# Kernel optimization log

Hardware: AMD Instinct MI355X
Metric: run time of the kernel (lower is better)

## Reference

```python
import jax, jax.numpy as jnp
import numpy as np

NEG_INF = -9e15


def setup_inputs() -> dict:
    key = jax.random.key(0)
    k1, k2, k3, k4, k5, k6 = jax.random.split(key, 6)
    B, N, F_IN, F_OUT = 16, 2048, 256, 128
    inputs = jax.random.normal(k1, (B, N, F_IN), dtype=jnp.float32)
    adj_matrix = jax.random.randint(k2, (B, N, N), 0, 2, dtype=jnp.int32)
    W = jax.random.normal(k3, (F_OUT, F_IN), dtype=jnp.float32) * (1.0 / np.sqrt(F_IN))
    b_W = jax.random.normal(k4, (F_OUT,), dtype=jnp.float32) * 0.02
    a = jax.random.normal(k5, (1, 2 * F_OUT), dtype=jnp.float32) * (1.0 / np.sqrt(2 * F_OUT))
    b_a = jax.random.normal(k6, (1,), dtype=jnp.float32) * 0.02
    return {"inputs": inputs, "adj_matrix": adj_matrix, "W": W, "b_W": b_W, "a": a, "b_a": b_a}


def reference(inputs, adj_matrix, W, b_W, a, b_a):
    # wh: [B, N, H]
    wh = jnp.einsum('bnf,hf->bnh', inputs, W) + b_W
    H = wh.shape[-1]
    # linear_self_W([wh_i, wh_j]) = a1.wh_i + a2.wh_j + b  (rank-1 linear over concat)
    a1 = a[0, :H]
    a2 = a[0, H:]
    src = jnp.einsum('bnh,h->bn', wh, a1)  # [B, N] contribution of row node i
    dst = jnp.einsum('bnh,h->bn', wh, a2)  # [B, N] contribution of col node j
    e = jax.nn.leaky_relu(src[:, :, None] + dst[:, None, :] + b_a[0], negative_slope=0.01)
    e = jnp.where(adj_matrix > 0, e, NEG_INF)
    att = jax.nn.softmax(e, axis=-1)  # dropout in eval mode = identity
    return jax.nn.elu(jnp.einsum('bij,bjh->bih', att, wh))
```

## Files before the change

kernel.cpp:

```cpp
#include <hip/hip_runtime.h>


#define BDIM 16
#define NDIM 2048
#define FIN 256
#define HDIM 128
#define LOG2E 1.4426950408889634f

typedef short short8 __attribute__((ext_vector_type(8)));
typedef float floatx4 __attribute__((ext_vector_type(4)));
typedef int intx4 __attribute__((ext_vector_type(4)));

__device__ __forceinline__ unsigned short f2bf(float x) {
    unsigned int u = __float_as_uint(x);
    unsigned int r = (u + 0x7fffu + ((u >> 16) & 1u)) >> 16;
    return (unsigned short)r;
}
__device__ __forceinline__ float bf2f(unsigned short s) {
    return __uint_as_float(((unsigned int)s) << 16);
}
__device__ __forceinline__ intx4 ldnt(const int* p) {
    return __builtin_nontemporal_load(reinterpret_cast<const intx4*>(p));
}

__global__ __launch_bounds__(256) void k_wh(const float* __restrict__ X,
                                            const float* __restrict__ W,
                                            const float* __restrict__ bW,
                                            const float* __restrict__ a,
                                            const float* __restrict__ ba_p,
                                            float* __restrict__ src,
                                            float* __restrict__ dst,
                                            unsigned short* __restrict__ whF) {
    __shared__ short lds[27648];
    short (*ah)[72] = (short(*)[72])lds;
    short (*al)[72] = (short(*)[72])(lds + 4608);
    short (*bh)[72] = (short(*)[72])(lds + 9216);
    short (*bl)[72] = (short(*)[72])(lds + 18432);
    short (*tb)[72] = (short(*)[72])lds;

    const int tid = threadIdx.x;
    const long row0 = (long)blockIdx.x * 64;
    const int w = tid >> 6, lane = tid & 63;
    const int lm = lane & 15, q = lane >> 4;
    const float ba0 = ba_p[0];

    float a1v[8], a2v[8], bwv[8];
    #pragma unroll
    for (int nt = 0; nt < 8; nt++) {
        a1v[nt] = a[nt * 16 + lm];
        a2v[nt] = a[HDIM + nt * 16 + lm];
        bwv[nt] = bW[nt * 16 + lm];
    }

    floatx4 acc[8];
    #pragma unroll
    for (int nt = 0; nt < 8; nt++) acc[nt] = (floatx4){0.f, 0.f, 0.f, 0.f};

    for (int k0 = 0; k0 < FIN; k0 += 64) {
        #pragma unroll
        for (int u = 0; u < 4; u++) {
            int idx = tid + u * 256;
            int r = idx >> 4, fc = (idx & 15) * 4;
            float4 v = *reinterpret_cast<const float4*>(X + (row0 + r) * FIN + k0 + fc);
            union { unsigned short s[4]; uint2 u2; } ph, pl;
            ph.s[0] = f2bf(v.x); pl.s[0] = f2bf(v.x - bf2f(ph.s[0]));
            ph.s[1] = f2bf(v.y); pl.s[1] = f2bf(v.y - bf2f(ph.s[1]));
            ph.s[2] = f2bf(v.z); pl.s[2] = f2bf(v.z - bf2f(ph.s[2]));
            ph.s[3] = f2bf(v.w); pl.s[3] = f2bf(v.w - bf2f(ph.s[3]));
            *reinterpret_cast<uint2*>(&ah[r][fc]) = ph.u2;
            *reinterpret_cast<uint2*>(&al[r][fc]) = pl.u2;
        }
        #pragma unroll
        for (int u = 0; u < 8; u++) {
            int idx = tid + u * 256;
            int hh = idx >> 4, fc = (idx & 15) * 4;
            float4 v = *reinterpret_cast<const float4*>(W + hh * FIN + k0 + fc);
            union { unsigned short s[4]; uint2 u2; } ph, pl;
            ph.s[0] = f2bf(v.x); pl.s[0] = f2bf(v.x - bf2f(ph.s[0]));
            ph.s[1] = f2bf(v.y); pl.s[1] = f2bf(v.y - bf2f(ph.s[1]));
            ph.s[2] = f2bf(v.z); pl.s[2] = f2bf(v.z - bf2f(ph.s[2]));
            ph.s[3] = f2bf(v.w); pl.s[3] = f2bf(v.w - bf2f(ph.s[3]));
            *reinterpret_cast<uint2*>(&bh[hh][fc]) = ph.u2;
            *reinterpret_cast<uint2*>(&bl[hh][fc]) = pl.u2;
        }
        __syncthreads();
        #pragma unroll
        for (int ks = 0; ks < 64; ks += 32) {
            short8 afh = *reinterpret_cast<const short8*>(&ah[w * 16 + lm][ks + q * 8]);
            short8 afl = *reinterpret_cast<const short8*>(&al[w * 16 + lm][ks + q * 8]);
            #pragma unroll
            for (int nt = 0; nt < 8; nt++) {
                short8 bfh = *reinterpret_cast<const short8*>(&bh[nt * 16 + lm][ks + q * 8]);
                short8 bfl = *reinterpret_cast<const short8*>(&bl[nt * 16 + lm][ks + q * 8]);
                acc[nt] = __builtin_amdgcn_mfma_f32_16x16x32_bf16(afh, bfh, acc[nt], 0, 0, 0);
                acc[nt] = __builtin_amdgcn_mfma_f32_16x16x32_bf16(afh, bfl, acc[nt], 0, 0, 0);
                acc[nt] = __builtin_amdgcn_mfma_f32_16x16x32_bf16(afl, bfh, acc[nt], 0, 0, 0);
            }
        }
        __syncthreads();
    }

    float s1[4] = {0.f, 0.f, 0.f, 0.f}, s2[4] = {0.f, 0.f, 0.f, 0.f};
    #pragma unroll
    for (int nt = 0; nt < 8; nt++) {
        #pragma unroll
        for (int r = 0; r < 4; r++) {
            float v = acc[nt][r] + bwv[nt];
            s1[r] += v * a1v[nt];
            s2[r] += v * a2v[nt];
            tb[nt * 16 + lm][w * 16 + q * 4 + r] = f2bf(v);
        }
    }
    #pragma unroll
    for (int r = 0; r < 4; r++) {
        #pragma unroll
        for (int o = 1; o < 16; o <<= 1) {
            s1[r] += __shfl_xor(s1[r], o);
            s2[r] += __shfl_xor(s2[r], o);
        }
    }
    if (lm == 0) {
        #pragma unroll
        for (int r = 0; r < 4; r++) {
            long row = row0 + w * 16 + q * 4 + r;
            src[row] = (s1[r] + ba0) * LOG2E;
            dst[row] = s2[r] * LOG2E;
        }
    }
    __syncthreads();
    const int b = (int)(row0 >> 11);
    const int jc0 = (int)((row0 & 2047) >> 5);
    const int f = tid >> 4;
    const int sub = tid & 15;
    const int jcrel = f >> 3, ht = f & 7;
    const size_t fbase = (((size_t)b * 64 + jc0 + jcrel) * 8 + ht) * 512;
    #pragma unroll
    for (int i = 0; i < 4; i++) {
        int l = sub * 4 + i;
        uint4 v = *reinterpret_cast<const uint4*>(&tb[ht * 16 + (l & 15)][jcrel * 32 + (l >> 4) * 8]);
        *reinterpret_cast<uint4*>(whF + fbase + l * 8) = v;
    }
}


#define MD_PRE(PW1, BK, HI)                                                    \
    do {                                                                       \
        md[PW1][0] = maskB[BK][0 + (HI)][wrow];                                \
        md[PW1][1] = maskB[BK][2 + (HI)][wrow];                                \
        md[PW1][2] = maskB[BK][4 + (HI)][wrow];                                \
        md[PW1][3] = maskB[BK][6 + (HI)][wrow];                                \
    } while (0)

#define ADJ_ISSUE(GNEXT, H)                                                    \
    do {                                                                       \
        _Pragma("unroll")                                                      \
        for (int r = 0; r < 8; r++) {                                          \
            const int* ap = adj +                                              \
                (size_t)(rowbase + cw * 16 + (H) * 8 + r) * NDIM +             \
                (GNEXT) * 256 + lane * 4;                                      \
            av[r] = ldnt(ap);                                                  \
        }                                                                      \
    } while (0)

#define ADJ_BALLOT(GNEXT, H)                                                   \
    do {                                                                       \
        _Pragma("unroll")                                                      \
        for (int r = 0; r < 8; r++) {                                          \
            unsigned long long b0 = __ballot(av[r][0] != 0);                   \
            unsigned long long b1 = __ballot(av[r][1] != 0);                   \
            unsigned long long b2 = __ballot(av[r][2] != 0);                   \
            unsigned long long b3 = __ballot(av[r][3] != 0);                   \
            if (lane < 8) {                                                    \
                unsigned long long bb = (lane < 2) ? b0                        \
                                        : (lane < 4) ? b1                      \
                                        : (lane < 6) ? b2 : b3;                \
                unsigned wv = (lane & 1) ? (unsigned)(bb >> 32) : (unsigned)bb;\
                maskB[(GNEXT) & 1][lane][cw * 16 + (H) * 8 + r] = wv;          \
            }                                                                  \
        }                                                                      \
    } while (0)

#define CHC(C)                                                                 \
    do {                                                                       \
        constexpr int PW = (C) & 1;                                            \
        const int T = g8 + (C);                                                \
        if (!(g8 == 56 && (C) == 7)) {                       \
            const float* dp = dstp + (T + 1) * 32;                             \
            d[PW ^ 1][0] = *reinterpret_cast<const floatx4*>(dp);              \
            d[PW ^ 1][1] = *reinterpret_cast<const floatx4*>(dp + 4);          \
            if ((C) < 7) {                                                     \
                MD_PRE(PW ^ 1, (g8 >> 3) & 1, (((C) + 1) & 4) ? 1 : 0);        \
            } else {                                                           \
                MD_PRE(PW ^ 1, ((g8 >> 3) + 1) & 1, 0);                        \
            }                                                                  \
        }                                                                      \
        const int base = 8 * ((C) & 3) + 2 * q;                                \
        short8 af;                                                             \
        _Pragma("unroll")                                                      \
        for (int j = 0; j < 8; j++) {                                          \
            float x = si + d[PW][j >> 2][j & 3];                               \
            x = fmaxf(x, 0.01f * x);               \
            float e2 = __builtin_amdgcn_exp2f(x);                              \
            unsigned bit = (md[PW][j & 3] >> (base + (j >> 2))) & 1u;          \
            float wgt = bit ? e2 : 0.f;                                        \
            lpart += wgt;                                                      \
            af[j] = (short)f2bf(wgt);                                          \
        }                                                                      \
        _Pragma("unroll")                                                      \
        for (int hj = 0; hj < 8; hj++) {                                       \
            short8 fb = *reinterpret_cast<const short8*>(                      \
                &whS[PW][hj * 512 + lane * 8]);                                \
            acc[hj] = __builtin_amdgcn_mfma_f32_16x16x32_bf16(af, fb,          \
                                                              acc[hj], 0, 0, 0); \
        }                                                                      \
    } while (0)

#define CHP(C)                                                                 \
    do {                                                                       \
        constexpr int PW = (C) & 1;                                            \
        const int T = g8 + (C);                                                \
        if (T + 2 < 64) {                   \
            const unsigned short* gp = gsrc + (size_t)(T + 2) * 4096;          \
            sr[PW][0] = *reinterpret_cast<const short8*>(gp);                  \
            sr[PW][1] = *reinterpret_cast<const short8*>(gp + 512);            \
        }                                                                      \
        if ((C) == 0 && g8 < 56) ADJ_ISSUE((g8 >> 3) + 1, 0);                  \
        if ((C) == 3 && g8 < 56) {                                             \
            ADJ_BALLOT((g8 >> 3) + 1, 0);                                      \
            ADJ_ISSUE((g8 >> 3) + 1, 1);                                       \
        }                                                                      \
        if ((C) == 6 && g8 < 56) ADJ_BALLOT((g8 >> 3) + 1, 1);                 \
        if (T + 1 < 64) {                 \
            *reinterpret_cast<short8*>(&whS[PW ^ 1][pofs]) = sr[PW ^ 1][0];    \
            *reinterpret_cast<short8*>(&whS[PW ^ 1][pofs + 512]) = sr[PW ^ 1][1]; \
        }                                                                      \
    } while (0)

#define ITER(C)                                                                \
    do {                                                                       \
        if (wave < 4) { CHC(C); } else { CHP(C); }                             \
        __syncthreads();                                                       \
    } while (0)

__global__ __launch_bounds__(512) void k_attn(const int* __restrict__ adj,
                                              const unsigned short* __restrict__ whF,
                                              const float* __restrict__ src,
                                              const float* __restrict__ dst,
                                              float* __restrict__ out) {
    __shared__ short whS[2][4096];
    __shared__ unsigned maskB[2][8][64];
    __shared__ float lred[64];
    __shared__ float linv_s[64];

    const int tid = threadIdx.x;
    const int bid = ((int)blockIdx.x & 7) * 64 + ((int)blockIdx.x >> 3);
    const int b = bid >> 5;
    const int i0 = (bid & 31) * 64;
    const int wave = tid >> 6, lane = tid & 63;
    const int cw = wave & 3;
    const int lm = lane & 15, q = lane >> 4;
    const int wrow = cw * 16 + lm;
    const int rowbase = b * NDIM + i0;

    const float si = src[rowbase + wrow];
    const float* dstp = dst + b * NDIM + q * 8;
    const unsigned short* gsrc =
        whF + (size_t)b * 64 * 8 * 512 + cw * 1024 + lane * 8;
    const int pofs = cw * 1024 + lane * 8;

    floatx4 acc[8];
    #pragma unroll
    for (int hj = 0; hj < 8; hj++) acc[hj] = (floatx4){0.f, 0.f, 0.f, 0.f};
    float lpart = 0.f;

    unsigned md[2][4];
    floatx4 d[2][2];
    short8 sr[2][2];
    intx4 av[8];

    if (wave >= 4) {
        short8 p0 = *reinterpret_cast<const short8*>(gsrc);
        short8 p1 = *reinterpret_cast<const short8*>(gsrc + 512);
        *reinterpret_cast<short8*>(&whS[0][pofs]) = p0;
        *reinterpret_cast<short8*>(&whS[0][pofs + 512]) = p1;
        sr[1][0] = *reinterpret_cast<const short8*>(gsrc + 4096);
        sr[1][1] = *reinterpret_cast<const short8*>(gsrc + 4096 + 512);
        ADJ_ISSUE(0, 0);
        ADJ_BALLOT(0, 0);
        ADJ_ISSUE(0, 1);
        ADJ_BALLOT(0, 1);
    } else {
        d[0][0] = *reinterpret_cast<const floatx4*>(dstp);
        d[0][1] = *reinterpret_cast<const floatx4*>(dstp + 4);
    }
    __syncthreads();
    if (wave < 4) MD_PRE(0, 0, 0);

    for (int g8 = 0; g8 < 64; g8 += 8) {
        ITER(0); ITER(1); ITER(2); ITER(3);
        ITER(4); ITER(5); ITER(6); ITER(7);
    }

    lpart += __shfl_xor(lpart, 16);
    lpart += __shfl_xor(lpart, 32);
    if (wave < 4 && q == 0) lred[cw * 16 + lm] = lpart;
    __syncthreads();
    if (tid < 64) {
        float l = lred[tid];
        linv_s[tid] = l > 0.f ? 1.f / l : 0.f;
    }
    __syncthreads();

    if (wave < 4) {
        #pragma unroll
        for (int r = 0; r < 4; r++) {
            int il = cw * 16 + q * 4 + r;
            float li = linv_s[il];
            size_t obase = ((size_t)(rowbase + il)) * HDIM + lm;
            #pragma unroll
            for (int hj = 0; hj < 8; hj++) {
                float x = acc[hj][r] * li;
                x = x > 0.f ? x : (__expf(x) - 1.f);
                out[obase + hj * 16] = x;
            }
        }
    }
}

extern "C" void kernel_launch(void* const* d_in, const int* in_sizes, int n_in,
                              void* d_out, int out_size, void* d_ws, size_t ws_size,
                              hipStream_t stream) {
    const float* X  = (const float*)d_in[0];
    const int* adj  = (const int*)d_in[1];
    const float* W  = (const float*)d_in[2];
    const float* bW = (const float*)d_in[3];
    const float* a  = (const float*)d_in[4];
    const float* ba = (const float*)d_in[5];
    float* out = (float*)d_out;

    float* srcv = (float*)d_ws;
    float* dstv = srcv + BDIM * NDIM;
    unsigned short* whF = (unsigned short*)(dstv + BDIM * NDIM);

    k_wh<<<BDIM * NDIM / 64, 256, 0, stream>>>(X, W, bW, a, ba, srcv, dstv, whF);
    k_attn<<<BDIM * (NDIM / 64), 512, 0, stream>>>(adj, whF, srcv, dstv, out);
}
```

Measured before the change: 427.8 us.

## Merge producer and consumer waves into unified 256-thread attention blocks

Replaces the warp-specialized design, where four waves load adjacency and wh tiles and four waves compute, with four waves that each prefetch their own wh slice, load and ballot the adjacency rows, and run the MFMA chunk. The block shrinks from 512 to 256 threads, and prefetch distance drops from two tiles to one using registers held across the compute. The mask shared array is padded to 65 columns to avoid bank conflicts. This removes idle producer waves and may allow more blocks per CU, but each wave now waits on its own memory latency with shallower prefetch.

```diff
diff --git a/kernel.cpp b/kernel.cpp
--- a/kernel.cpp
+++ b/kernel.cpp
@@ -156,7 +156,7 @@
         _Pragma("unroll")                                                      \
         for (int r = 0; r < 8; r++) {                                          \
             const int* ap = adj +                                              \
-                (size_t)(rowbase + cw * 16 + (H) * 8 + r) * NDIM +             \
+                (size_t)(rowbase + wave * 16 + (H) * 8 + r) * NDIM +           \
                 (GNEXT) * 256 + lane * 4;                                      \
             av[r] = ldnt(ap);                                                  \
         }                                                                      \
@@ -175,16 +175,28 @@
                                         : (lane < 4) ? b1                      \
                                         : (lane < 6) ? b2 : b3;                \
                 unsigned wv = (lane & 1) ? (unsigned)(bb >> 32) : (unsigned)bb;\
-                maskB[(GNEXT) & 1][lane][cw * 16 + (H) * 8 + r] = wv;          \
+                maskB[(GNEXT) & 1][lane][wave * 16 + (H) * 8 + r] = wv;        \
             }                                                                  \
         }                                                                      \
     } while (0)
 
-#define CHC(C)                                                                 \
+#define CH(C)                                                                  \
     do {                                                                       \
         constexpr int PW = (C) & 1;                                            \
         const int T = g8 + (C);                                                \
-        if (!(g8 == 56 && (C) == 7)) {                       \
+        short8 s0, s1;                                                         \
+        if (T < 63) {                 \
+            const unsigned short* gp = gsrc + (size_t)(T + 1) * 4096;          \
+            s0 = *reinterpret_cast<const short8*>(gp);                         \
+            s1 = *reinterpret_cast<const short8*>(gp + 512);                   \
+        }                                                                      \
+        if ((C) == 0 && g8 < 56) ADJ_ISSUE((g8 >> 3) + 1, 0);                  \
+        if ((C) == 3 && g8 < 56) {                                             \
+            ADJ_BALLOT((g8 >> 3) + 1, 0);                                      \
+            ADJ_ISSUE((g8 >> 3) + 1, 1);                                       \
+        }                                                                      \
+        if ((C) == 6 && g8 < 56) ADJ_BALLOT((g8 >> 3) + 1, 1);                 \
+        if (T < 63) {                   \
             const float* dp = dstp + (T + 1) * 32;                             \
             d[PW ^ 1][0] = *reinterpret_cast<const floatx4*>(dp);              \
             d[PW ^ 1][1] = *reinterpret_cast<const floatx4*>(dp + 4);          \
@@ -213,42 +225,20 @@
             acc[hj] = __builtin_amdgcn_mfma_f32_16x16x32_bf16(af, fb,          \
                                                               acc[hj], 0, 0, 0); \
         }                                                                      \
-    } while (0)
-
-#define CHP(C)                                                                 \
-    do {                                                                       \
-        constexpr int PW = (C) & 1;                                            \
-        const int T = g8 + (C);                                                \
-        if (T + 2 < 64) {                   \
-            const unsigned short* gp = gsrc + (size_t)(T + 2) * 4096;          \
-            sr[PW][0] = *reinterpret_cast<const short8*>(gp);                  \
-            sr[PW][1] = *reinterpret_cast<const short8*>(gp + 512);            \
-        }                                                                      \
-        if ((C) == 0 && g8 < 56) ADJ_ISSUE((g8 >> 3) + 1, 0);                  \
-        if ((C) == 3 && g8 < 56) {                                             \
-            ADJ_BALLOT((g8 >> 3) + 1, 0);                                      \
-            ADJ_ISSUE((g8 >> 3) + 1, 1);                                       \
-        }                                                                      \
-        if ((C) == 6 && g8 < 56) ADJ_BALLOT((g8 >> 3) + 1, 1);                 \
-        if (T + 1 < 64) {                 \
-            *reinterpret_cast<short8*>(&whS[PW ^ 1][pofs]) = sr[PW ^ 1][0];    \
-            *reinterpret_cast<short8*>(&whS[PW ^ 1][pofs + 512]) = sr[PW ^ 1][1]; \
-        }                                                                      \
-    } while (0)
-
-#define ITER(C)                                                                \
-    do {                                                                       \
-        if (wave < 4) { CHC(C); } else { CHP(C); }                             \
+        if (T < 63) {          \
+            *reinterpret_cast<short8*>(&whS[PW ^ 1][pofs]) = s0;               \
+            *reinterpret_cast<short8*>(&whS[PW ^ 1][pofs + 512]) = s1;         \
+        }                                                                      \
         __syncthreads();                                                       \
     } while (0)
 
-__global__ __launch_bounds__(512) void k_attn(const int* __restrict__ adj,
+__global__ __launch_bounds__(256) void k_attn(const int* __restrict__ adj,
                                               const unsigned short* __restrict__ whF,
                                               const float* __restrict__ src,
                                               const float* __restrict__ dst,
                                               float* __restrict__ out) {
     __shared__ short whS[2][4096];
-    __shared__ unsigned maskB[2][8][64];
+    __shared__ unsigned maskB[2][8][65];
     __shared__ float lred[64];
     __shared__ float linv_s[64];
 
@@ -257,16 +247,15 @@
     const int b = bid >> 5;
     const int i0 = (bid & 31) * 64;
     const int wave = tid >> 6, lane = tid & 63;
-    const int cw = wave & 3;
     const int lm = lane & 15, q = lane >> 4;
-    const int wrow = cw * 16 + lm;
+    const int wrow = wave * 16 + lm;
     const int rowbase = b * NDIM + i0;
 
     const float si = src[rowbase + wrow];
     const float* dstp = dst + b * NDIM + q * 8;
     const unsigned short* gsrc =
-        whF + (size_t)b * 64 * 8 * 512 + cw * 1024 + lane * 8;
-    const int pofs = cw * 1024 + lane * 8;
+        whF + (size_t)b * 64 * 8 * 512 + wave * 1024 + lane * 8;
+    const int pofs = wave * 1024 + lane * 8;
 
     floatx4 acc[8];
     #pragma unroll
@@ -275,35 +264,31 @@
 
     unsigned md[2][4];
     floatx4 d[2][2];
-    short8 sr[2][2];
     intx4 av[8];
 
-    if (wave >= 4) {
+    {
         short8 p0 = *reinterpret_cast<const short8*>(gsrc);
         short8 p1 = *reinterpret_cast<const short8*>(gsrc + 512);
         *reinterpret_cast<short8*>(&whS[0][pofs]) = p0;
         *reinterpret_cast<short8*>(&whS[0][pofs + 512]) = p1;
-        sr[1][0] = *reinterpret_cast<const short8*>(gsrc + 4096);
-        sr[1][1] = *reinterpret_cast<const short8*>(gsrc + 4096 + 512);
-        ADJ_ISSUE(0, 0);
-        ADJ_BALLOT(0, 0);
-        ADJ_ISSUE(0, 1);
-        ADJ_BALLOT(0, 1);
-    } else {
-        d[0][0] = *reinterpret_cast<const floatx4*>(dstp);
-        d[0][1] = *reinterpret_cast<const floatx4*>(dstp + 4);
-    }
+    }
+    ADJ_ISSUE(0, 0);
+    ADJ_BALLOT(0, 0);
+    ADJ_ISSUE(0, 1);
+    ADJ_BALLOT(0, 1);
+    d[0][0] = *reinterpret_cast<const floatx4*>(dstp);
+    d[0][1] = *reinterpret_cast<const floatx4*>(dstp + 4);
     __syncthreads();
-    if (wave < 4) MD_PRE(0, 0, 0);
+    MD_PRE(0, 0, 0);
 
     for (int g8 = 0; g8 < 64; g8 += 8) {
-        ITER(0); ITER(1); ITER(2); ITER(3);
-        ITER(4); ITER(5); ITER(6); ITER(7);
+        CH(0); CH(1); CH(2); CH(3);
+        CH(4); CH(5); CH(6); CH(7);
     }
 
     lpart += __shfl_xor(lpart, 16);
     lpart += __shfl_xor(lpart, 32);
-    if (wave < 4 && q == 0) lred[cw * 16 + lm] = lpart;
+    if (q == 0) lred[wrow] = lpart;
     __syncthreads();
     if (tid < 64) {
         float l = lred[tid];
@@ -311,18 +296,16 @@
     }
     __syncthreads();
 
-    if (wave < 4) {
-        #pragma unroll
-        for (int r = 0; r < 4; r++) {
-            int il = cw * 16 + q * 4 + r;
-            float li = linv_s[il];
-            size_t obase = ((size_t)(rowbase + il)) * HDIM + lm;
-            #pragma unroll
-            for (int hj = 0; hj < 8; hj++) {
-                float x = acc[hj][r] * li;
-                x = x > 0.f ? x : (__expf(x) - 1.f);
-                out[obase + hj * 16] = x;
-            }
+    #pragma unroll
+    for (int r = 0; r < 4; r++) {
+        int il = wave * 16 + q * 4 + r;
+        float li = linv_s[il];
+        size_t obase = ((size_t)(rowbase + il)) * HDIM + lm;
+        #pragma unroll
+        for (int hj = 0; hj < 8; hj++) {
+            float x = acc[hj][r] * li;
+            x = x > 0.f ? x : (__expf(x) - 1.f);
+            out[obase + hj * 16] = x;
         }
     }
 }
@@ -343,5 +326,5 @@
     unsigned short* whF = (unsigned short*)(dstv + BDIM * NDIM);
 
     k_wh<<<BDIM * NDIM / 64, 256, 0, stream>>>(X, W, bW, a, ba, srcv, dstv, whF);
-    k_attn<<<BDIM * (NDIM / 64), 512, 0, stream>>>(adj, whF, srcv, dstv, out);
-}
+    k_attn<<<BDIM * (NDIM / 64), 256, 0, stream>>>(adj, whF, srcv, dstv, out);
+}
```

New measurement: 413.7 us. 1.03x faster.
